# Performance work log

Measured on AMD Instinct MI355X. Metric: run time of the kernel, lower is better.

Reference implementation:

```python
import jax, jax.numpy as jnp
import numpy as np

B, T, D, H = 4, 2048, 384, 6
HD = D // H  # 64
HALF = HD // 2


def setup_inputs() -> dict:
    key = jax.random.key(0)
    k0, k1, k2 = jax.random.split(key, 3)
    x = jax.random.normal(k0, (B, T, D), jnp.float32)
    attn_bias = jnp.zeros((1, 1, T, T), jnp.float32)  # additive SDPA bias
    # standard RoPE tables: [T, HD/2]
    inv_freq = 1.0 / (10000.0 ** (np.arange(HALF, dtype=np.float32) / HALF))
    ang = np.arange(T, dtype=np.float32)[:, None] * inv_freq[None, :]
    cos = jnp.asarray(np.cos(ang), jnp.float32)
    sin = jnp.asarray(np.sin(ang), jnp.float32)
    w_qkv = jax.random.normal(k1, (D, 3 * D), jnp.float32) * (D ** -0.5)
    w_proj = jax.random.normal(k2, (D, D), jnp.float32) * (D ** -0.5)
    return {"x": x, "attn_bias": attn_bias, "cos": cos, "sin": sin,
            "w_qkv": w_qkv, "w_proj": w_proj}


def _apply_rope(x, cos, sin):
    # x: [b, h, t, hd]; cos/sin: [t, hd/2] -> rotate-half RoPE
    half = x.shape[-1] // 2
    x1, x2 = x[..., :half], x[..., half:]
    c = cos[None, None, :, :]
    s = sin[None, None, :, :]
    return jnp.concatenate([x1 * c - x2 * s, x2 * c + x1 * s], axis=-1)


def reference(x, attn_bias, cos, sin, w_qkv, w_proj):
    b, t, _ = x.shape
    qkv = (x @ w_qkv).reshape(b, t, 3, H, HD)  # fused QKV projection
    q = jnp.transpose(qkv[:, :, 0], (0, 2, 1, 3))  # [b,h,t,hd]
    k = jnp.transpose(qkv[:, :, 1], (0, 2, 1, 3))
    v = jnp.transpose(qkv[:, :, 2], (0, 2, 1, 3))
    q = _apply_rope(q, cos, sin)
    k = _apply_rope(k, cos, sin)
    scale = 1.0 / jnp.sqrt(jnp.asarray(HD, x.dtype))
    scores = jnp.einsum("bhqd,bhkd->bhqk", q, k) * scale + attn_bias
    attn = jax.nn.softmax(scores, axis=-1)
    out = jnp.einsum("bhqk,bhkd->bhqd", attn, v)
    out = jnp.transpose(out, (0, 2, 1, 3)).reshape(b, t, H * HD)
    return out @ w_proj
```

## Files before the change

### kernel.cpp

```cpp
#include <hip/hip_runtime.h>
#include <hip/hip_bf16.h>

#define BB   4
#define TT   2048
#define DDIM 384
#define HH   6
#define HD   64
#define BT   (BB*TT)
#define QKVC (3*DDIM)

#define QSCALE 0.18033688011112042f
#define LOG2E  1.4426950408889634f

typedef __attribute__((ext_vector_type(4))) short short4v;
typedef __attribute__((ext_vector_type(8))) short short8v;
typedef __attribute__((ext_vector_type(4))) float float4v;
typedef unsigned short u16;

static __device__ __forceinline__ u16 f2bu(float f) {
    __hip_bfloat16 h = __float2bfloat16(f);
    return __builtin_bit_cast(u16, h);
}
static __device__ __forceinline__ unsigned pk2(float lo, float hi) {
    return (unsigned)f2bu(lo) | ((unsigned)f2bu(hi) << 16);
}
static __device__ __forceinline__ short8v frag4(uint4 v) {
    return __builtin_bit_cast(short8v, v);
}
static __device__ __forceinline__ short8v ld_frag(const u16* p) {
    short4v a = *(const short4v*)p;
    short4v b = *(const short4v*)(p + 4);
    return __builtin_shufflevector(a, b, 0, 1, 2, 3, 4, 5, 6, 7);
}
static __device__ __forceinline__ void st8(u16* p, uint4 v) {
    *(uint2*)p       = make_uint2(v.x, v.y);
    *(uint2*)(p + 4) = make_uint2(v.z, v.w);
}
static __device__ __forceinline__ void pl32swap(unsigned &a, unsigned &b) {
    auto r = __builtin_amdgcn_permlane32_swap(a, b, false, false);
    a = r[0]; b = r[1];
}
static __device__ __forceinline__ void pl16swap(unsigned &a, unsigned &b) {
    auto r = __builtin_amdgcn_permlane16_swap(a, b, false, false);
    a = r[0]; b = r[1];
}

#define MFMA16(a, b, c) __builtin_amdgcn_mfma_f32_16x16x32_bf16((a), (b), (c), 0, 0, 0)

__global__ __launch_bounds__(256) void prep_kernel(
    const float* __restrict__ wqkv, const float* __restrict__ wproj,
    const float* __restrict__ x, const float* __restrict__ bias,
    u16* __restrict__ wqkvT, u16* __restrict__ wprojT,
    u16* __restrict__ xb, unsigned* __restrict__ flag)
{
    const int bid = blockIdx.x;
    const int t = threadIdx.x;
    if (bid >= 912) {
        const float* gp = bias + (size_t)(bid - 912) * 4096 + (size_t)t * 16;
        unsigned acc = 0;
        #pragma unroll
        for (int u = 0; u < 4; ++u) {
            float4 v = *(const float4*)(gp + 4 * u);
            acc |= (__builtin_bit_cast(unsigned, v.x) & 0x7fffffffu);
            acc |= (__builtin_bit_cast(unsigned, v.y) & 0x7fffffffu);
            acc |= (__builtin_bit_cast(unsigned, v.z) & 0x7fffffffu);
            acc |= (__builtin_bit_cast(unsigned, v.w) & 0x7fffffffu);
        }
        if (acc) atomicOr(flag, 1u);
        return;
    }
    if (bid >= 144) {
        size_t base = (size_t)(bid - 144) * 4096 + (size_t)t * 16;
        const float* gp = x + base;
        __align__(16) u16 tmp[16];
        #pragma unroll
        for (int u = 0; u < 4; ++u) {
            float4 v = *(const float4*)(gp + 4 * u);
            tmp[4 * u + 0] = f2bu(v.x); tmp[4 * u + 1] = f2bu(v.y);
            tmp[4 * u + 2] = f2bu(v.z); tmp[4 * u + 3] = f2bu(v.w);
        }
        *(uint4*)(xb + base)     = *(const uint4*)tmp;
        *(uint4*)(xb + base + 8) = *(const uint4*)(tmp + 8);
        return;
    }
    const float* in; u16* out; int K, C, c0, k0;
    if (bid < 108) { in = wqkv;  out = wqkvT;  K = DDIM; C = QKVC;
                     c0 = (bid % 18) * 64; k0 = (bid / 18) * 64; }
    else           { int b2 = bid - 108; in = wproj; out = wprojT; K = DDIM; C = DDIM;
                     c0 = (b2 % 6) * 64; k0 = (b2 / 6) * 64; }
    __shared__ float tr[64][65];
    {
        int kr = t >> 2, cb = (t & 3) * 16;
        const float* gp = in + (size_t)(k0 + kr) * C + c0 + cb;
        #pragma unroll
        for (int u = 0; u < 4; ++u) {
            float4 v = *(const float4*)(gp + 4 * u);
            tr[cb + 4 * u + 0][kr] = v.x;
            tr[cb + 4 * u + 1][kr] = v.y;
            tr[cb + 4 * u + 2][kr] = v.z;
            tr[cb + 4 * u + 3][kr] = v.w;
        }
    }
    __syncthreads();
    {
        int c = t >> 2, kb = (t & 3) * 16;
        __align__(16) u16 tmp[16];
        #pragma unroll
        for (int u = 0; u < 16; ++u) tmp[u] = f2bu(tr[c][kb + u]);
        u16* op = out + (size_t)(c0 + c) * K + k0 + kb;
        *(uint4*)op       = *(const uint4*)tmp;
        *(uint4*)(op + 8) = *(const uint4*)(tmp + 8);
    }
}

__global__ __launch_bounds__(256, 3) void qkv_rope_kernel(
    const u16* __restrict__ xb, const u16* __restrict__ wt,
    const float* __restrict__ cs, const float* __restrict__ sn,
    u16* __restrict__ qb, u16* __restrict__ kb, u16* __restrict__ vtb)
{
    __shared__ __align__(16) u16 ws[64][392];
    const int t = threadIdx.x;
    const int wv = t >> 6, lane = t & 63, quad = lane >> 4, lo = lane & 15;
    const int r0 = blockIdx.y * 64, c0 = blockIdx.x * 64;

    {
        const uint4* src = (const uint4*)(wt + (size_t)c0 * DDIM);
        #pragma unroll
        for (int u = 0; u < 12; ++u) {
            int idx = t + u * 256;
            int f = idx * 8;
            int row = f / DDIM, col = f % DDIM;
            *(uint4*)&ws[row][col] = src[idx];
        }
    }
    const u16* arow = xb + (size_t)(r0 + 16 * wv + lo) * DDIM + quad * 8;
    uint4 af[12];
    #pragma unroll
    for (int kf = 0; kf < 12; ++kf)
        af[kf] = *(const uint4*)(arow + kf * 32);
    __syncthreads();

    float4v acc[4] = {};
    #pragma unroll
    for (int kf = 0; kf < 12; ++kf) {
        short8v a = frag4(af[kf]);
        #pragma unroll
        for (int nt = 0; nt < 4; ++nt) {
            short8v b = ld_frag(&ws[nt * 16 + lo][kf * 32 + quad * 8]);
            acc[nt] = MFMA16(a, b, acc[nt]);
        }
    }

    const int sec = blockIdx.x / 6;
    const int h   = blockIdx.x % 6;
    const int rbase = r0 + 16 * wv + 4 * quad;
    const int bidx  = r0 >> 11;
    const int tbase = rbase & (TT - 1);

    if (sec == 2) {
        #pragma unroll
        for (int nt = 0; nt < 4; ++nt) {
            int d = nt * 16 + lo;
            unsigned a0 = pk2(acc[nt][0], acc[nt][1]);
            unsigned a1 = pk2(acc[nt][2], acc[nt][3]);
            u16* gp = vtb + ((size_t)(bidx * HH + h) * HD + d) * TT + tbase;
            *(uint2*)gp = make_uint2(a0, a1);
        }
    } else {
        u16* dst = (sec == 0) ? qb : kb;
        const float scl = (sec == 0) ? QSCALE : 1.0f;
        #pragma unroll
        for (int np = 0; np < 2; ++np) {
            #pragma unroll
            for (int r = 0; r < 4; ++r) {
                int tpos = tbase + r;
                int ci = np * 16 + lo;
                float cv = cs[tpos * 32 + ci];
                float sv = sn[tpos * 32 + ci];
                float x1 = acc[np][r], x2 = acc[np + 2][r];
                u16* gp = dst + ((size_t)(bidx * HH + h) * TT + tpos) * HD;
                gp[ci]      = f2bu((x1 * cv - x2 * sv) * scl);
                gp[ci + 32] = f2bu((x2 * cv + x1 * sv) * scl);
            }
        }
    }
}

__global__ __launch_bounds__(256, 2) void attn_ksplit_kernel(
    const u16* __restrict__ qb, const u16* __restrict__ kb, const u16* __restrict__ vtb,
    const unsigned* __restrict__ flag, u16* __restrict__ ob)
{
    if (*flag != 0u) return;

    __shared__ __align__(16) float red_o[2][64][68];
    __shared__ float red_l[4][64];

    const int t = threadIdx.x;
    const int wv = t >> 6, lane = t & 63, quad = lane >> 4, lo = lane & 15;
    const int bh = blockIdx.x;
    const int b = bh / HH, h = bh % HH;
    const int q0 = blockIdx.y * 64;

    short8v aq[4][2];
    #pragma unroll
    for (int g = 0; g < 4; ++g) {
        const u16* qp = qb + ((size_t)bh * TT + q0 + g * 16 + lo) * HD + quad * 8;
        aq[g][0] = frag4(*(const uint4*)qp);
        aq[g][1] = frag4(*(const uint4*)(qp + 32));
    }

    const u16* kbase = kb + ((size_t)bh * TT + lo) * HD + quad * 8;
    const u16* vbase = vtb + ((size_t)bh * HD + lo) * TT + quad * 8;

    uint4 kq[4][2], vq[4][2];
    {
        const size_t ko = (size_t)wv * 64 * HD;
        const size_t vo = (size_t)wv * 64;
        #pragma unroll
        for (int nt = 0; nt < 4; ++nt) {
            kq[nt][0] = *(const uint4*)(kbase + ko + (size_t)nt * 16 * HD);
            kq[nt][1] = *(const uint4*)(kbase + ko + (size_t)nt * 16 * HD + 32);
        }
        #pragma unroll
        for (int dt = 0; dt < 4; ++dt) {
            vq[dt][0] = *(const uint4*)(vbase + (size_t)dt * 16 * TT + vo);
            vq[dt][1] = *(const uint4*)(vbase + (size_t)dt * 16 * TT + vo + 32);
        }
    }

    float4v oacc[4][4] = {};
    float lacc[4] = {0.f, 0.f, 0.f, 0.f};

    for (int j = 0; j < 8; ++j) {
        const int ktn = (j < 7) ? (wv + 4 * (j + 1)) : wv;
        const size_t kno = (size_t)ktn * 64 * HD;
        const size_t vno = (size_t)ktn * 64;

        #pragma unroll
        for (int g = 0; g < 4; ++g) {
            float4v s[4] = {};
            #pragma unroll
            for (int nt = 0; nt < 4; ++nt)
                s[nt] = MFMA16(frag4(kq[nt][0]), aq[g][0], s[nt]);
            #pragma unroll
            for (int nt = 0; nt < 4; ++nt)
                s[nt] = MFMA16(frag4(kq[nt][1]), aq[g][1], s[nt]);
            if (g == 3) {
                #pragma unroll
                for (int nt = 0; nt < 4; ++nt) {
                    kq[nt][0] = *(const uint4*)(kbase + kno + (size_t)nt * 16 * HD);
                    kq[nt][1] = *(const uint4*)(kbase + kno + (size_t)nt * 16 * HD + 32);
                }
            }

            unsigned w[8];
            #pragma unroll
            for (int nt = 0; nt < 4; ++nt) {
                float p0 = __builtin_amdgcn_exp2f(s[nt][0]);
                float p1 = __builtin_amdgcn_exp2f(s[nt][1]);
                float p2 = __builtin_amdgcn_exp2f(s[nt][2]);
                float p3 = __builtin_amdgcn_exp2f(s[nt][3]);
                lacc[g] += (p0 + p1) + (p2 + p3);
                w[2 * nt]     = pk2(p0, p1);
                w[2 * nt + 1] = pk2(p2, p3);
            }

            pl32swap(w[0], w[2]); pl16swap(w[0], w[2]);
            pl32swap(w[1], w[3]); pl16swap(w[1], w[3]);
            pl32swap(w[4], w[6]); pl16swap(w[4], w[6]);
            pl32swap(w[5], w[7]); pl16swap(w[5], w[7]);
            short8v pa0 = frag4(make_uint4(w[0], w[1], w[2], w[3]));
            short8v pa1 = frag4(make_uint4(w[4], w[5], w[6], w[7]));

            #pragma unroll
            for (int dt = 0; dt < 4; ++dt)
                oacc[g][dt] = MFMA16(pa0, frag4(vq[dt][0]), oacc[g][dt]);
            #pragma unroll
            for (int dt = 0; dt < 4; ++dt)
                oacc[g][dt] = MFMA16(pa1, frag4(vq[dt][1]), oacc[g][dt]);
            if (g == 3) {
                #pragma unroll
                for (int dt = 0; dt < 4; ++dt) {
                    vq[dt][0] = *(const uint4*)(vbase + (size_t)dt * 16 * TT + vno);
                    vq[dt][1] = *(const uint4*)(vbase + (size_t)dt * 16 * TT + vno + 32);
                }
            }
        }
    }

    #pragma unroll
    for (int g = 0; g < 4; ++g) {
        lacc[g] += __shfl_xor(lacc[g], 16);
        lacc[g] += __shfl_xor(lacc[g], 32);
    }
    if (quad == 0) {
        #pragma unroll
        for (int g = 0; g < 4; ++g) red_l[wv][g * 16 + lo] = lacc[g];
    }
    float* slot0 = &red_o[0][0][0] + (size_t)lane * 68;
    float* slot1 = &red_o[1][0][0] + (size_t)lane * 68;
    if (wv == 1 || wv == 3) {
        float* sp = (wv == 1) ? slot0 : slot1;
        #pragma unroll
        for (int g = 0; g < 4; ++g)
            #pragma unroll
            for (int dt = 0; dt < 4; ++dt)
                *(float4v*)(sp + (g * 4 + dt) * 4) = oacc[g][dt];
    }
    __syncthreads();
    if (wv == 0 || wv == 2) {
        float* sp = (wv == 0) ? slot0 : slot1;
        #pragma unroll
        for (int g = 0; g < 4; ++g)
            #pragma unroll
            for (int dt = 0; dt < 4; ++dt)
                oacc[g][dt] += *(const float4v*)(sp + (g * 4 + dt) * 4);
    }
    __syncthreads();
    if (wv == 2) {
        #pragma unroll
        for (int g = 0; g < 4; ++g)
            #pragma unroll
            for (int dt = 0; dt < 4; ++dt)
                *(float4v*)(slot1 + (g * 4 + dt) * 4) = oacc[g][dt];
    }
    __syncthreads();
    if (wv == 0) {
        #pragma unroll
        for (int g = 0; g < 4; ++g) {
            #pragma unroll
            for (int dt = 0; dt < 4; ++dt)
                oacc[g][dt] += *(const float4v*)(slot1 + (g * 4 + dt) * 4);
            float lt = red_l[0][g * 16 + lo] + red_l[1][g * 16 + lo]
                     + red_l[2][g * 16 + lo] + red_l[3][g * 16 + lo];
            #pragma unroll
            for (int r = 0; r < 4; ++r) {
                float lr = __shfl(lt, 4 * quad + r);
                float inv = 1.f / lr;
                u16* gp = ob + ((size_t)b * TT + q0 + g * 16 + 4 * quad + r) * DDIM
                             + h * HD + lo;
                #pragma unroll
                for (int dt = 0; dt < 4; ++dt)
                    gp[dt * 16] = f2bu(oacc[g][dt][r] * inv);
            }
        }
    }
}

__global__ __launch_bounds__(256, 4) void attn_bias_kernel(
    const u16* __restrict__ qb, const u16* __restrict__ kb, const u16* __restrict__ vtb,
    const float* __restrict__ bias, const unsigned* __restrict__ flag,
    u16* __restrict__ ob)
{
    if (*flag == 0u) return;

    __shared__ __align__(16) u16 ks[2][64][68];
    __shared__ __align__(16) u16 vt[2][64][68];

    const int t = threadIdx.x;
    const int wv = t >> 6, lane = t & 63, quad = lane >> 4, lo = lane & 15;
    const int bh = blockIdx.x;
    const int b = bh / HH, h = bh % HH;
    const int q0 = blockIdx.y * 64;
    const int qrow = q0 + 16 * wv + lo;

    const u16* qbase = qb + ((size_t)bh * TT + qrow) * HD + quad * 8;
    short8v aq0 = frag4(*(const uint4*)qbase);
    short8v aq1 = frag4(*(const uint4*)(qbase + 32));

    const int sr = t >> 3, sd = (t & 7) * 8;
    const u16* kbbase = kb + (size_t)bh * TT * HD;
    const u16* vtbase = vtb + (size_t)bh * HD * TT;
    const float* brow = bias + (size_t)qrow * TT + 4 * quad;

    st8(&ks[0][sr][sd],      *(const uint4*)(kbbase + (size_t)sr * HD + sd));
    st8(&ks[0][sr + 32][sd], *(const uint4*)(kbbase + (size_t)(sr + 32) * HD + sd));
    st8(&vt[0][sr][sd],      *(const uint4*)(vtbase + (size_t)sr * TT + sd));
    st8(&vt[0][sr + 32][sd], *(const uint4*)(vtbase + (size_t)(sr + 32) * TT + sd));
    float4 bcur[4];
    #pragma unroll
    for (int nt = 0; nt < 4; ++nt) bcur[nt] = *(const float4*)(brow + nt * 16);
    __syncthreads();

    float4v oacc[4] = {};
    float lacc[4] = {0.f, 0.f, 0.f, 0.f};

    for (int kt = 0; kt < TT / 64; ++kt) {
        const int cur = kt & 1, nxt = cur ^ 1;
        const int kn = (kt < 31 ? kt + 1 : 31) * 64;

        uint4 kp0 = *(const uint4*)(kbbase + (size_t)(kn + sr) * HD + sd);
        uint4 kp1 = *(const uint4*)(kbbase + (size_t)(kn + sr + 32) * HD + sd);
        uint4 vp0 = *(const uint4*)(vtbase + (size_t)sr * TT + kn + sd);
        uint4 vp1 = *(const uint4*)(vtbase + (size_t)(sr + 32) * TT + kn + sd);
        float4 bnxt[4];
        #pragma unroll
        for (int nt = 0; nt < 4; ++nt) bnxt[nt] = *(const float4*)(brow + kn + nt * 16);

        float4v s[4] = {};
        #pragma unroll
        for (int kf = 0; kf < 2; ++kf) {
            #pragma unroll
            for (int nt = 0; nt < 4; ++nt) {
                short8v kfr = ld_frag(&ks[cur][nt * 16 + lo][kf * 32 + quad * 8]);
                s[nt] = MFMA16(kfr, (kf ? aq1 : aq0), s[nt]);
            }
        }

        unsigned w[8];
        #pragma unroll
        for (int nt = 0; nt < 4; ++nt) {
            float p0 = __builtin_amdgcn_exp2f(fmaf(bcur[nt].x, LOG2E, s[nt][0]));
            float p1 = __builtin_amdgcn_exp2f(fmaf(bcur[nt].y, LOG2E, s[nt][1]));
            float p2 = __builtin_amdgcn_exp2f(fmaf(bcur[nt].z, LOG2E, s[nt][2]));
            float p3 = __builtin_amdgcn_exp2f(fmaf(bcur[nt].w, LOG2E, s[nt][3]));
            lacc[nt] += (p0 + p1) + (p2 + p3);
            w[2 * nt]     = pk2(p0, p1);
            w[2 * nt + 1] = pk2(p2, p3);
        }

        pl32swap(w[0], w[2]); pl16swap(w[0], w[2]);
        pl32swap(w[1], w[3]); pl16swap(w[1], w[3]);
        pl32swap(w[4], w[6]); pl16swap(w[4], w[6]);
        pl32swap(w[5], w[7]); pl16swap(w[5], w[7]);
        short8v pa0 = frag4(make_uint4(w[0], w[1], w[2], w[3]));
        short8v pa1 = frag4(make_uint4(w[4], w[5], w[6], w[7]));

        #pragma unroll
        for (int kf = 0; kf < 2; ++kf) {
            #pragma unroll
            for (int dt = 0; dt < 4; ++dt) {
                short8v bv = ld_frag(&vt[cur][dt * 16 + lo][kf * 32 + quad * 8]);
                oacc[dt] = MFMA16((kf ? pa1 : pa0), bv, oacc[dt]);
            }
        }

        st8(&ks[nxt][sr][sd], kp0);
        st8(&ks[nxt][sr + 32][sd], kp1);
        st8(&vt[nxt][sr][sd], vp0);
        st8(&vt[nxt][sr + 32][sd], vp1);
        #pragma unroll
        for (int nt = 0; nt < 4; ++nt) bcur[nt] = bnxt[nt];
        __syncthreads();
    }

    float l = (lacc[0] + lacc[1]) + (lacc[2] + lacc[3]);
    l += __shfl_xor(l, 16);
    l += __shfl_xor(l, 32);
    #pragma unroll
    for (int r = 0; r < 4; ++r) {
        float lr = __shfl(l, 4 * quad + r);
        float inv = 1.f / lr;
        u16* gp = ob + ((size_t)b * TT + q0 + 16 * wv + 4 * quad + r) * DDIM + h * HD + lo;
        #pragma unroll
        for (int dt = 0; dt < 4; ++dt)
            gp[dt * 16] = f2bu(oacc[dt][r] * inv);
    }
}

__global__ __launch_bounds__(256, 3) void proj_kernel(
    const u16* __restrict__ o, const u16* __restrict__ wt, float* __restrict__ out)
{
    __shared__ __align__(16) u16 ws[64][392];
    const int t = threadIdx.x;
    const int wv = t >> 6, lane = t & 63, quad = lane >> 4, lo = lane & 15;
    const int r0 = blockIdx.y * 64, c0 = blockIdx.x * 64;

    {
        const uint4* src = (const uint4*)(wt + (size_t)c0 * DDIM);
        #pragma unroll
        for (int u = 0; u < 12; ++u) {
            int idx = t + u * 256;
            int f = idx * 8;
            int row = f / DDIM, col = f % DDIM;
            *(uint4*)&ws[row][col] = src[idx];
        }
    }
    const u16* arow = o + (size_t)(r0 + 16 * wv + lo) * DDIM + quad * 8;
    uint4 af[12];
    #pragma unroll
    for (int kf = 0; kf < 12; ++kf)
        af[kf] = *(const uint4*)(arow + kf * 32);
    __syncthreads();

    float4v acc[4] = {};
    #pragma unroll
    for (int kf = 0; kf < 12; ++kf) {
        short8v a = frag4(af[kf]);
        #pragma unroll
        for (int nt = 0; nt < 4; ++nt) {
            short8v b = ld_frag(&ws[nt * 16 + lo][kf * 32 + quad * 8]);
            acc[nt] = MFMA16(a, b, acc[nt]);
        }
    }
    #pragma unroll
    for (int r = 0; r < 4; ++r) {
        float* gp = out + (size_t)(r0 + 16 * wv + 4 * quad + r) * DDIM + c0;
        #pragma unroll
        for (int nt = 0; nt < 4; ++nt)
            gp[nt * 16 + lo] = acc[nt][r];
    }
}

extern "C" void kernel_launch(void* const* d_in, const int* in_sizes, int n_in,
                              void* d_out, int out_size, void* d_ws, size_t ws_size,
                              hipStream_t stream) {
    const float* x     = (const float*)d_in[0];
    const float* bias  = (const float*)d_in[1];
    const float* cs    = (const float*)d_in[2];
    const float* sn    = (const float*)d_in[3];
    const float* wqkv  = (const float*)d_in[4];
    const float* wproj = (const float*)d_in[5];
    float* out = (float*)d_out;

    u16* wqkvT  = (u16*)d_ws;
    u16* wprojT = wqkvT + (size_t)QKVC * DDIM;
    u16* qb     = wprojT + (size_t)DDIM * DDIM;
    u16* kb     = qb + (size_t)BB * HH * TT * HD;
    u16* vtb    = kb + (size_t)BB * HH * TT * HD;
    u16* ob     = vtb + (size_t)BB * HH * TT * HD;
    u16* xb     = ob + (size_t)BT * DDIM;
    unsigned* flag = (unsigned*)(xb + (size_t)BT * DDIM);

    hipMemsetAsync(flag, 0, sizeof(unsigned), stream);
    prep_kernel<<<dim3(144 + BT * DDIM / 4096 + TT * TT / 4096), 256, 0, stream>>>(
        wqkv, wproj, x, bias, wqkvT, wprojT, xb, flag);
    qkv_rope_kernel<<<dim3(QKVC / 64, BT / 64), 256, 0, stream>>>(
        xb, wqkvT, cs, sn, qb, kb, vtb);
    attn_ksplit_kernel<<<dim3(BB * HH, TT / 64), 256, 0, stream>>>(
        qb, kb, vtb, flag, ob);
    attn_bias_kernel<<<dim3(BB * HH, TT / 64), 256, 0, stream>>>(
        qb, kb, vtb, bias, flag, ob);
    proj_kernel<<<dim3(DDIM / 64, BT / 64), 256, 0, stream>>>(ob, wprojT, out);
}
```

Measured before the change: 171.7 us.

## Fuse fp32-to-bf16 weight and input conversion into GEMM kernels, merge attention kernels

Removes the separate prep kernel. The QKV and projection kernels now read fp32 weights and x directly, transposing and converting them to bf16 while staging into shared memory or registers. The bias-check blocks are appended to the QKV grid, and the two attention kernels are merged into one that branches on the flag, which saves a launch. In exchange, every GEMM block re-converts its weight tile from strided fp32 loads, so global traffic per block goes up.

```diff
diff --git a/kernel.cpp b/kernel.cpp
--- a/kernel.cpp
+++ b/kernel.cpp
@@ -47,16 +47,39 @@
 
 #define MFMA16(a, b, c) __builtin_amdgcn_mfma_f32_16x16x32_bf16((a), (b), (c), 0, 0, 0)
 
-__global__ __launch_bounds__(256) void prep_kernel(
-    const float* __restrict__ wqkv, const float* __restrict__ wproj,
-    const float* __restrict__ x, const float* __restrict__ bias,
-    u16* __restrict__ wqkvT, u16* __restrict__ wprojT,
-    u16* __restrict__ xb, unsigned* __restrict__ flag)
+static __device__ __forceinline__ void stage_wT(
+    u16 (*ws)[392], const float* __restrict__ w, int C, int c0, int t)
+{
+    const int c = t & 63;
+    const int kb0 = t >> 6;
+    #pragma unroll
+    for (int u = 0; u < 12; ++u) {
+        int k = (kb0 + 4 * u) * 8;
+        const float* wp = w + (size_t)k * C + c0 + c;
+        float v0 = wp[0];
+        float v1 = wp[(size_t)1 * C];
+        float v2 = wp[(size_t)2 * C];
+        float v3 = wp[(size_t)3 * C];
+        float v4 = wp[(size_t)4 * C];
+        float v5 = wp[(size_t)5 * C];
+        float v6 = wp[(size_t)6 * C];
+        float v7 = wp[(size_t)7 * C];
+        uint4 pv = make_uint4(pk2(v0, v1), pk2(v2, v3), pk2(v4, v5), pk2(v6, v7));
+        *(uint4*)&ws[c][k] = pv;
+    }
+}
+
+__global__ __launch_bounds__(256, 3) void qkv_fused_kernel(
+    const float* __restrict__ x, const float* __restrict__ wqkv,
+    const float* __restrict__ bias,
+    const float* __restrict__ cs, const float* __restrict__ sn,
+    u16* __restrict__ qb, u16* __restrict__ kb, u16* __restrict__ vtb,
+    unsigned* __restrict__ flag)
 {
     const int bid = blockIdx.x;
     const int t = threadIdx.x;
-    if (bid >= 912) {
-        const float* gp = bias + (size_t)(bid - 912) * 4096 + (size_t)t * 16;
+    if (bid >= 2304) {
+        const float* gp = bias + (size_t)(bid - 2304) * 4096 + (size_t)t * 16;
         unsigned acc = 0;
         #pragma unroll
         for (int u = 0; u < 4; ++u) {
@@ -69,75 +92,23 @@
         if (acc) atomicOr(flag, 1u);
         return;
     }
-    if (bid >= 144) {
-        size_t base = (size_t)(bid - 144) * 4096 + (size_t)t * 16;
-        const float* gp = x + base;
-        __align__(16) u16 tmp[16];
-        #pragma unroll
-        for (int u = 0; u < 4; ++u) {
-            float4 v = *(const float4*)(gp + 4 * u);
-            tmp[4 * u + 0] = f2bu(v.x); tmp[4 * u + 1] = f2bu(v.y);
-            tmp[4 * u + 2] = f2bu(v.z); tmp[4 * u + 3] = f2bu(v.w);
-        }
-        *(uint4*)(xb + base)     = *(const uint4*)tmp;
-        *(uint4*)(xb + base + 8) = *(const uint4*)(tmp + 8);
-        return;
-    }
-    const float* in; u16* out; int K, C, c0, k0;
-    if (bid < 108) { in = wqkv;  out = wqkvT;  K = DDIM; C = QKVC;
-                     c0 = (bid % 18) * 64; k0 = (bid / 18) * 64; }
-    else           { int b2 = bid - 108; in = wproj; out = wprojT; K = DDIM; C = DDIM;
-                     c0 = (b2 % 6) * 64; k0 = (b2 / 6) * 64; }
-    __shared__ float tr[64][65];
-    {
-        int kr = t >> 2, cb = (t & 3) * 16;
-        const float* gp = in + (size_t)(k0 + kr) * C + c0 + cb;
-        #pragma unroll
-        for (int u = 0; u < 4; ++u) {
-            float4 v = *(const float4*)(gp + 4 * u);
-            tr[cb + 4 * u + 0][kr] = v.x;
-            tr[cb + 4 * u + 1][kr] = v.y;
-            tr[cb + 4 * u + 2][kr] = v.z;
-            tr[cb + 4 * u + 3][kr] = v.w;
-        }
-    }
-    __syncthreads();
-    {
-        int c = t >> 2, kb = (t & 3) * 16;
-        __align__(16) u16 tmp[16];
-        #pragma unroll
-        for (int u = 0; u < 16; ++u) tmp[u] = f2bu(tr[c][kb + u]);
-        u16* op = out + (size_t)(c0 + c) * K + k0 + kb;
-        *(uint4*)op       = *(const uint4*)tmp;
-        *(uint4*)(op + 8) = *(const uint4*)(tmp + 8);
-    }
-}
-
-__global__ __launch_bounds__(256, 3) void qkv_rope_kernel(
-    const u16* __restrict__ xb, const u16* __restrict__ wt,
-    const float* __restrict__ cs, const float* __restrict__ sn,
-    u16* __restrict__ qb, u16* __restrict__ kb, u16* __restrict__ vtb)
-{
+
     __shared__ __align__(16) u16 ws[64][392];
-    const int t = threadIdx.x;
     const int wv = t >> 6, lane = t & 63, quad = lane >> 4, lo = lane & 15;
-    const int r0 = blockIdx.y * 64, c0 = blockIdx.x * 64;
-
-    {
-        const uint4* src = (const uint4*)(wt + (size_t)c0 * DDIM);
-        #pragma unroll
-        for (int u = 0; u < 12; ++u) {
-            int idx = t + u * 256;
-            int f = idx * 8;
-            int row = f / DDIM, col = f % DDIM;
-            *(uint4*)&ws[row][col] = src[idx];
-        }
-    }
-    const u16* arow = xb + (size_t)(r0 + 16 * wv + lo) * DDIM + quad * 8;
+    const int c0 = (bid % 18) * 64;
+    const int r0 = (bid / 18) * 64;
+
+    stage_wT(ws, wqkv, QKVC, c0, t);
+
+    const float* arow = x + (size_t)(r0 + 16 * wv + lo) * DDIM + quad * 8;
     uint4 af[12];
     #pragma unroll
-    for (int kf = 0; kf < 12; ++kf)
-        af[kf] = *(const uint4*)(arow + kf * 32);
+    for (int kf = 0; kf < 12; ++kf) {
+        float4 a0 = *(const float4*)(arow + kf * 32);
+        float4 a1 = *(const float4*)(arow + kf * 32 + 4);
+        af[kf] = make_uint4(pk2(a0.x, a0.y), pk2(a0.z, a0.w),
+                            pk2(a1.x, a1.y), pk2(a1.z, a1.w));
+    }
     __syncthreads();
 
     float4v acc[4] = {};
@@ -151,8 +122,9 @@
         }
     }
 
-    const int sec = blockIdx.x / 6;
-    const int h   = blockIdx.x % 6;
+    const int cb = bid % 18;
+    const int sec = cb / 6;
+    const int h   = cb % 6;
     const int rbase = r0 + 16 * wv + 4 * quad;
     const int bidx  = r0 >> 11;
     const int tbase = rbase & (TT - 1);
@@ -186,14 +158,12 @@
     }
 }
 
-__global__ __launch_bounds__(256, 2) void attn_ksplit_kernel(
+__global__ __launch_bounds__(256, 2) void attn_unified_kernel(
     const u16* __restrict__ qb, const u16* __restrict__ kb, const u16* __restrict__ vtb,
-    const unsigned* __restrict__ flag, u16* __restrict__ ob)
+    const float* __restrict__ bias, const unsigned* __restrict__ flag,
+    u16* __restrict__ ob)
 {
-    if (*flag != 0u) return;
-
-    __shared__ __align__(16) float red_o[2][64][68];
-    __shared__ float red_l[4][64];
+    __shared__ __align__(16) u16 smem[17920];
 
     const int t = threadIdx.x;
     const int wv = t >> 6, lane = t & 63, quad = lane >> 4, lo = lane & 15;
@@ -201,66 +171,215 @@
     const int b = bh / HH, h = bh % HH;
     const int q0 = blockIdx.y * 64;
 
-    short8v aq[4][2];
-    #pragma unroll
-    for (int g = 0; g < 4; ++g) {
-        const u16* qp = qb + ((size_t)bh * TT + q0 + g * 16 + lo) * HD + quad * 8;
-        aq[g][0] = frag4(*(const uint4*)qp);
-        aq[g][1] = frag4(*(const uint4*)(qp + 32));
-    }
-
-    const u16* kbase = kb + ((size_t)bh * TT + lo) * HD + quad * 8;
-    const u16* vbase = vtb + ((size_t)bh * HD + lo) * TT + quad * 8;
-
-    uint4 kq[4][2], vq[4][2];
+    if (*flag == 0u) {
+        float* red_o = (float*)smem;
+        float* red_l = (float*)(smem + 17408);
+
+        short8v aq[4][2];
+        #pragma unroll
+        for (int g = 0; g < 4; ++g) {
+            const u16* qp = qb + ((size_t)bh * TT + q0 + g * 16 + lo) * HD + quad * 8;
+            aq[g][0] = frag4(*(const uint4*)qp);
+            aq[g][1] = frag4(*(const uint4*)(qp + 32));
+        }
+
+        const u16* kbase = kb + ((size_t)bh * TT + lo) * HD + quad * 8;
+        const u16* vbase = vtb + ((size_t)bh * HD + lo) * TT + quad * 8;
+
+        uint4 kq[4][2], vq[4][2];
+        {
+            const size_t ko = (size_t)wv * 64 * HD;
+            const size_t vo = (size_t)wv * 64;
+            #pragma unroll
+            for (int nt = 0; nt < 4; ++nt) {
+                kq[nt][0] = *(const uint4*)(kbase + ko + (size_t)nt * 16 * HD);
+                kq[nt][1] = *(const uint4*)(kbase + ko + (size_t)nt * 16 * HD + 32);
+            }
+            #pragma unroll
+            for (int dt = 0; dt < 4; ++dt) {
+                vq[dt][0] = *(const uint4*)(vbase + (size_t)dt * 16 * TT + vo);
+                vq[dt][1] = *(const uint4*)(vbase + (size_t)dt * 16 * TT + vo + 32);
+            }
+        }
+
+        float4v oacc[4][4] = {};
+        float lacc[4] = {0.f, 0.f, 0.f, 0.f};
+
+        for (int j = 0; j < 8; ++j) {
+            const int ktn = (j < 7) ? (wv + 4 * (j + 1)) : wv;
+            const size_t kno = (size_t)ktn * 64 * HD;
+            const size_t vno = (size_t)ktn * 64;
+
+            #pragma unroll
+            for (int g = 0; g < 4; ++g) {
+                float4v s[4] = {};
+                #pragma unroll
+                for (int nt = 0; nt < 4; ++nt)
+                    s[nt] = MFMA16(frag4(kq[nt][0]), aq[g][0], s[nt]);
+                #pragma unroll
+                for (int nt = 0; nt < 4; ++nt)
+                    s[nt] = MFMA16(frag4(kq[nt][1]), aq[g][1], s[nt]);
+                if (g == 3) {
+                    #pragma unroll
+                    for (int nt = 0; nt < 4; ++nt) {
+                        kq[nt][0] = *(const uint4*)(kbase + kno + (size_t)nt * 16 * HD);
+                        kq[nt][1] = *(const uint4*)(kbase + kno + (size_t)nt * 16 * HD + 32);
+                    }
+                }
+
+                unsigned w[8];
+                #pragma unroll
+                for (int nt = 0; nt < 4; ++nt) {
+                    float p0 = __builtin_amdgcn_exp2f(s[nt][0]);
+                    float p1 = __builtin_amdgcn_exp2f(s[nt][1]);
+                    float p2 = __builtin_amdgcn_exp2f(s[nt][2]);
+                    float p3 = __builtin_amdgcn_exp2f(s[nt][3]);
+                    lacc[g] += (p0 + p1) + (p2 + p3);
+                    w[2 * nt]     = pk2(p0, p1);
+                    w[2 * nt + 1] = pk2(p2, p3);
+                }
+
+                pl32swap(w[0], w[2]); pl16swap(w[0], w[2]);
+                pl32swap(w[1], w[3]); pl16swap(w[1], w[3]);
+                pl32swap(w[4], w[6]); pl16swap(w[4], w[6]);
+                pl32swap(w[5], w[7]); pl16swap(w[5], w[7]);
+                short8v pa0 = frag4(make_uint4(w[0], w[1], w[2], w[3]));
+                short8v pa1 = frag4(make_uint4(w[4], w[5], w[6], w[7]));
+
+                #pragma unroll
+                for (int dt = 0; dt < 4; ++dt)
+                    oacc[g][dt] = MFMA16(pa0, frag4(vq[dt][0]), oacc[g][dt]);
+                #pragma unroll
+                for (int dt = 0; dt < 4; ++dt)
+                    oacc[g][dt] = MFMA16(pa1, frag4(vq[dt][1]), oacc[g][dt]);
+                if (g == 3) {
+                    #pragma unroll
+                    for (int dt = 0; dt < 4; ++dt) {
+                        vq[dt][0] = *(const uint4*)(vbase + (size_t)dt * 16 * TT + vno);
+                        vq[dt][1] = *(const uint4*)(vbase + (size_t)dt * 16 * TT + vno + 32);
+                    }
+                }
+            }
+        }
+
+        #pragma unroll
+        for (int g = 0; g < 4; ++g) {
+            lacc[g] += __shfl_xor(lacc[g], 16);
+            lacc[g] += __shfl_xor(lacc[g], 32);
+        }
+        if (quad == 0) {
+            #pragma unroll
+            for (int g = 0; g < 4; ++g) red_l[wv * 64 + g * 16 + lo] = lacc[g];
+        }
+        float* slot0 = red_o + (size_t)lane * 68;
+        float* slot1 = red_o + 64 * 68 + (size_t)lane * 68;
+        if (wv == 1 || wv == 3) {
+            float* sp = (wv == 1) ? slot0 : slot1;
+            #pragma unroll
+            for (int g = 0; g < 4; ++g)
+                #pragma unroll
+                for (int dt = 0; dt < 4; ++dt)
+                    *(float4v*)(sp + (g * 4 + dt) * 4) = oacc[g][dt];
+        }
+        __syncthreads();
+        if (wv == 0 || wv == 2) {
+            float* sp = (wv == 0) ? slot0 : slot1;
+            #pragma unroll
+            for (int g = 0; g < 4; ++g)
+                #pragma unroll
+                for (int dt = 0; dt < 4; ++dt)
+                    oacc[g][dt] += *(const float4v*)(sp + (g * 4 + dt) * 4);
+        }
+        __syncthreads();
+        if (wv == 2) {
+            #pragma unroll
+            for (int g = 0; g < 4; ++g)
+                #pragma unroll
+                for (int dt = 0; dt < 4; ++dt)
+                    *(float4v*)(slot1 + (g * 4 + dt) * 4) = oacc[g][dt];
+        }
+        __syncthreads();
+        if (wv == 0) {
+            #pragma unroll
+            for (int g = 0; g < 4; ++g) {
+                #pragma unroll
+                for (int dt = 0; dt < 4; ++dt)
+                    oacc[g][dt] += *(const float4v*)(slot1 + (g * 4 + dt) * 4);
+                float lt = red_l[0 * 64 + g * 16 + lo] + red_l[1 * 64 + g * 16 + lo]
+                         + red_l[2 * 64 + g * 16 + lo] + red_l[3 * 64 + g * 16 + lo];
+                #pragma unroll
+                for (int r = 0; r < 4; ++r) {
+                    float lr = __shfl(lt, 4 * quad + r);
+                    float inv = 1.f / lr;
+                    u16* gp = ob + ((size_t)b * TT + q0 + g * 16 + 4 * quad + r) * DDIM
+                                 + h * HD + lo;
+                    #pragma unroll
+                    for (int dt = 0; dt < 4; ++dt)
+                        gp[dt * 16] = f2bu(oacc[g][dt][r] * inv);
+                }
+            }
+        }
+        return;
+    }
+
     {
-        const size_t ko = (size_t)wv * 64 * HD;
-        const size_t vo = (size_t)wv * 64;
-        #pragma unroll
-        for (int nt = 0; nt < 4; ++nt) {
-            kq[nt][0] = *(const uint4*)(kbase + ko + (size_t)nt * 16 * HD);
-            kq[nt][1] = *(const uint4*)(kbase + ko + (size_t)nt * 16 * HD + 32);
-        }
-        #pragma unroll
-        for (int dt = 0; dt < 4; ++dt) {
-            vq[dt][0] = *(const uint4*)(vbase + (size_t)dt * 16 * TT + vo);
-            vq[dt][1] = *(const uint4*)(vbase + (size_t)dt * 16 * TT + vo + 32);
-        }
-    }
-
-    float4v oacc[4][4] = {};
-    float lacc[4] = {0.f, 0.f, 0.f, 0.f};
-
-    for (int j = 0; j < 8; ++j) {
-        const int ktn = (j < 7) ? (wv + 4 * (j + 1)) : wv;
-        const size_t kno = (size_t)ktn * 64 * HD;
-        const size_t vno = (size_t)ktn * 64;
-
-        #pragma unroll
-        for (int g = 0; g < 4; ++g) {
+        typedef u16 (*lds_t)[64][68];
+        lds_t ks = (lds_t)smem;
+        lds_t vt = (lds_t)(smem + 8704);
+
+        const int qrow = q0 + 16 * wv + lo;
+        const u16* qbase = qb + ((size_t)bh * TT + qrow) * HD + quad * 8;
+        short8v aq0 = frag4(*(const uint4*)qbase);
+        short8v aq1 = frag4(*(const uint4*)(qbase + 32));
+
+        const int sr = t >> 3, sd = (t & 7) * 8;
+        const u16* kbbase = kb + (size_t)bh * TT * HD;
+        const u16* vtbase = vtb + (size_t)bh * HD * TT;
+        const float* brow = bias + (size_t)qrow * TT + 4 * quad;
+
+        st8(&ks[0][sr][sd],      *(const uint4*)(kbbase + (size_t)sr * HD + sd));
+        st8(&ks[0][sr + 32][sd], *(const uint4*)(kbbase + (size_t)(sr + 32) * HD + sd));
+        st8(&vt[0][sr][sd],      *(const uint4*)(vtbase + (size_t)sr * TT + sd));
+        st8(&vt[0][sr + 32][sd], *(const uint4*)(vtbase + (size_t)(sr + 32) * TT + sd));
+        float4 bcur[4];
+        #pragma unroll
+        for (int nt = 0; nt < 4; ++nt) bcur[nt] = *(const float4*)(brow + nt * 16);
+        __syncthreads();
+
+        float4v oacc[4] = {};
+        float lacc[4] = {0.f, 0.f, 0.f, 0.f};
+
+        for (int kt = 0; kt < TT / 64; ++kt) {
+            const int cur = kt & 1, nxt = cur ^ 1;
+            const int kn = (kt < 31 ? kt + 1 : 31) * 64;
+
+            uint4 kp0 = *(const uint4*)(kbbase + (size_t)(kn + sr) * HD + sd);
+            uint4 kp1 = *(const uint4*)(kbbase + (size_t)(kn + sr + 32) * HD + sd);
+            uint4 vp0 = *(const uint4*)(vtbase + (size_t)sr * TT + kn + sd);
+            uint4 vp1 = *(const uint4*)(vtbase + (size_t)(sr + 32) * TT + kn + sd);
+            float4 bnxt[4];
+            #pragma unroll
+            for (int nt = 0; nt < 4; ++nt)
+                bnxt[nt] = *(const float4*)(brow + kn + nt * 16);
+
             float4v s[4] = {};
             #pragma unroll
-            for (int nt = 0; nt < 4; ++nt)
-                s[nt] = MFMA16(frag4(kq[nt][0]), aq[g][0], s[nt]);
-            #pragma unroll
-            for (int nt = 0; nt < 4; ++nt)
-                s[nt] = MFMA16(frag4(kq[nt][1]), aq[g][1], s[nt]);
-            if (g == 3) {
+            for (int kf = 0; kf < 2; ++kf) {
                 #pragma unroll
                 for (int nt = 0; nt < 4; ++nt) {
-                    kq[nt][0] = *(const uint4*)(kbase + kno + (size_t)nt * 16 * HD);
-                    kq[nt][1] = *(const uint4*)(kbase + kno + (size_t)nt * 16 * HD + 32);
+                    short8v kfr = ld_frag(&ks[cur][nt * 16 + lo][kf * 32 + quad * 8]);
+                    s[nt] = MFMA16(kfr, (kf ? aq1 : aq0), s[nt]);
                 }
             }
 
             unsigned w[8];
             #pragma unroll
             for (int nt = 0; nt < 4; ++nt) {
-                float p0 = __builtin_amdgcn_exp2f(s[nt][0]);
-                float p1 = __builtin_amdgcn_exp2f(s[nt][1]);
-                float p2 = __builtin_amdgcn_exp2f(s[nt][2]);
-                float p3 = __builtin_amdgcn_exp2f(s[nt][3]);
-                lacc[g] += (p0 + p1) + (p2 + p3);
+                float p0 = __builtin_amdgcn_exp2f(fmaf(bcur[nt].x, LOG2E, s[nt][0]));
+                float p1 = __builtin_amdgcn_exp2f(fmaf(bcur[nt].y, LOG2E, s[nt][1]));
+                float p2 = __builtin_amdgcn_exp2f(fmaf(bcur[nt].z, LOG2E, s[nt][2]));
+                float p3 = __builtin_amdgcn_exp2f(fmaf(bcur[nt].w, LOG2E, s[nt][3]));
+                lacc[nt] += (p0 + p1) + (p2 + p3);
                 w[2 * nt]     = pk2(p0, p1);
                 w[2 * nt + 1] = pk2(p2, p3);
             }
@@ -273,209 +392,50 @@
             short8v pa1 = frag4(make_uint4(w[4], w[5], w[6], w[7]));
 
             #pragma unroll
+            for (int kf = 0; kf < 2; ++kf) {
+                #pragma unroll
+                for (int dt = 0; dt < 4; ++dt) {
+                    short8v bv = ld_frag(&vt[cur][dt * 16 + lo][kf * 32 + quad * 8]);
+                    oacc[dt] = MFMA16((kf ? pa1 : pa0), bv, oacc[dt]);
+                }
+            }
+
+            st8(&ks[nxt][sr][sd], kp0);
+            st8(&ks[nxt][sr + 32][sd], kp1);
+            st8(&vt[nxt][sr][sd], vp0);
+            st8(&vt[nxt][sr + 32][sd], vp1);
+            #pragma unroll
+            for (int nt = 0; nt < 4; ++nt) bcur[nt] = bnxt[nt];
+            __syncthreads();
+        }
+
+        float l = (lacc[0] + lacc[1]) + (lacc[2] + lacc[3]);
+        l += __shfl_xor(l, 16);
+        l += __shfl_xor(l, 32);
+        #pragma unroll
+        for (int r = 0; r < 4; ++r) {
+            float lr = __shfl(l, 4 * quad + r);
+            float inv = 1.f / lr;
+            u16* gp = ob + ((size_t)b * TT + q0 + 16 * wv + 4 * quad + r) * DDIM
+                         + h * HD + lo;
+            #pragma unroll
             for (int dt = 0; dt < 4; ++dt)
-                oacc[g][dt] = MFMA16(pa0, frag4(vq[dt][0]), oacc[g][dt]);
-            #pragma unroll
-            for (int dt = 0; dt < 4; ++dt)
-                oacc[g][dt] = MFMA16(pa1, frag4(vq[dt][1]), oacc[g][dt]);
-            if (g == 3) {
-                #pragma unroll
-                for (int dt = 0; dt < 4; ++dt) {
-                    vq[dt][0] = *(const uint4*)(vbase + (size_t)dt * 16 * TT + vno);
-                    vq[dt][1] = *(const uint4*)(vbase + (size_t)dt * 16 * TT + vno + 32);
-                }
-            }
-        }
-    }
-
-    #pragma unroll
-    for (int g = 0; g < 4; ++g) {
-        lacc[g] += __shfl_xor(lacc[g], 16);
-        lacc[g] += __shfl_xor(lacc[g], 32);
-    }
-    if (quad == 0) {
-        #pragma unroll
-        for (int g = 0; g < 4; ++g) red_l[wv][g * 16 + lo] = lacc[g];
-    }
-    float* slot0 = &red_o[0][0][0] + (size_t)lane * 68;
-    float* slot1 = &red_o[1][0][0] + (size_t)lane * 68;
-    if (wv == 1 || wv == 3) {
-        float* sp = (wv == 1) ? slot0 : slot1;
-        #pragma unroll
-        for (int g = 0; g < 4; ++g)
-            #pragma unroll
-            for (int dt = 0; dt < 4; ++dt)
-                *(float4v*)(sp + (g * 4 + dt) * 4) = oacc[g][dt];
-    }
-    __syncthreads();
-    if (wv == 0 || wv == 2) {
-        float* sp = (wv == 0) ? slot0 : slot1;
-        #pragma unroll
-        for (int g = 0; g < 4; ++g)
-            #pragma unroll
-            for (int dt = 0; dt < 4; ++dt)
-                oacc[g][dt] += *(const float4v*)(sp + (g * 4 + dt) * 4);
-    }
-    __syncthreads();
-    if (wv == 2) {
-        #pragma unroll
-        for (int g = 0; g < 4; ++g)
-            #pragma unroll
-            for (int dt = 0; dt < 4; ++dt)
-                *(float4v*)(slot1 + (g * 4 + dt) * 4) = oacc[g][dt];
-    }
-    __syncthreads();
-    if (wv == 0) {
-        #pragma unroll
-        for (int g = 0; g < 4; ++g) {
-            #pragma unroll
-            for (int dt = 0; dt < 4; ++dt)
-                oacc[g][dt] += *(const float4v*)(slot1 + (g * 4 + dt) * 4);
-            float lt = red_l[0][g * 16 + lo] + red_l[1][g * 16 + lo]
-                     + red_l[2][g * 16 + lo] + red_l[3][g * 16 + lo];
-            #pragma unroll
-            for (int r = 0; r < 4; ++r) {
-                float lr = __shfl(lt, 4 * quad + r);
-                float inv = 1.f / lr;
-                u16* gp = ob + ((size_t)b * TT + q0 + g * 16 + 4 * quad + r) * DDIM
-                             + h * HD + lo;
-                #pragma unroll
-                for (int dt = 0; dt < 4; ++dt)
-                    gp[dt * 16] = f2bu(oacc[g][dt][r] * inv);
-            }
-        }
-    }
-}
-
-__global__ __launch_bounds__(256, 4) void attn_bias_kernel(
-    const u16* __restrict__ qb, const u16* __restrict__ kb, const u16* __restrict__ vtb,
-    const float* __restrict__ bias, const unsigned* __restrict__ flag,
-    u16* __restrict__ ob)
-{
-    if (*flag == 0u) return;
-
-    __shared__ __align__(16) u16 ks[2][64][68];
-    __shared__ __align__(16) u16 vt[2][64][68];
-
-    const int t = threadIdx.x;
-    const int wv = t >> 6, lane = t & 63, quad = lane >> 4, lo = lane & 15;
-    const int bh = blockIdx.x;
-    const int b = bh / HH, h = bh % HH;
-    const int q0 = blockIdx.y * 64;
-    const int qrow = q0 + 16 * wv + lo;
-
-    const u16* qbase = qb + ((size_t)bh * TT + qrow) * HD + quad * 8;
-    short8v aq0 = frag4(*(const uint4*)qbase);
-    short8v aq1 = frag4(*(const uint4*)(qbase + 32));
-
-    const int sr = t >> 3, sd = (t & 7) * 8;
-    const u16* kbbase = kb + (size_t)bh * TT * HD;
-    const u16* vtbase = vtb + (size_t)bh * HD * TT;
-    const float* brow = bias + (size_t)qrow * TT + 4 * quad;
-
-    st8(&ks[0][sr][sd],      *(const uint4*)(kbbase + (size_t)sr * HD + sd));
-    st8(&ks[0][sr + 32][sd], *(const uint4*)(kbbase + (size_t)(sr + 32) * HD + sd));
-    st8(&vt[0][sr][sd],      *(const uint4*)(vtbase + (size_t)sr * TT + sd));
-    st8(&vt[0][sr + 32][sd], *(const uint4*)(vtbase + (size_t)(sr + 32) * TT + sd));
-    float4 bcur[4];
-    #pragma unroll
-    for (int nt = 0; nt < 4; ++nt) bcur[nt] = *(const float4*)(brow + nt * 16);
-    __syncthreads();
-
-    float4v oacc[4] = {};
-    float lacc[4] = {0.f, 0.f, 0.f, 0.f};
-
-    for (int kt = 0; kt < TT / 64; ++kt) {
-        const int cur = kt & 1, nxt = cur ^ 1;
-        const int kn = (kt < 31 ? kt + 1 : 31) * 64;
-
-        uint4 kp0 = *(const uint4*)(kbbase + (size_t)(kn + sr) * HD + sd);
-        uint4 kp1 = *(const uint4*)(kbbase + (size_t)(kn + sr + 32) * HD + sd);
-        uint4 vp0 = *(const uint4*)(vtbase + (size_t)sr * TT + kn + sd);
-        uint4 vp1 = *(const uint4*)(vtbase + (size_t)(sr + 32) * TT + kn + sd);
-        float4 bnxt[4];
-        #pragma unroll
-        for (int nt = 0; nt < 4; ++nt) bnxt[nt] = *(const float4*)(brow + kn + nt * 16);
-
-        float4v s[4] = {};
-        #pragma unroll
-        for (int kf = 0; kf < 2; ++kf) {
-            #pragma unroll
-            for (int nt = 0; nt < 4; ++nt) {
-                short8v kfr = ld_frag(&ks[cur][nt * 16 + lo][kf * 32 + quad * 8]);
-                s[nt] = MFMA16(kfr, (kf ? aq1 : aq0), s[nt]);
-            }
-        }
-
-        unsigned w[8];
-        #pragma unroll
-        for (int nt = 0; nt < 4; ++nt) {
-            float p0 = __builtin_amdgcn_exp2f(fmaf(bcur[nt].x, LOG2E, s[nt][0]));
-            float p1 = __builtin_amdgcn_exp2f(fmaf(bcur[nt].y, LOG2E, s[nt][1]));
-            float p2 = __builtin_amdgcn_exp2f(fmaf(bcur[nt].z, LOG2E, s[nt][2]));
-            float p3 = __builtin_amdgcn_exp2f(fmaf(bcur[nt].w, LOG2E, s[nt][3]));
-            lacc[nt] += (p0 + p1) + (p2 + p3);
-            w[2 * nt]     = pk2(p0, p1);
-            w[2 * nt + 1] = pk2(p2, p3);
-        }
-
-        pl32swap(w[0], w[2]); pl16swap(w[0], w[2]);
-        pl32swap(w[1], w[3]); pl16swap(w[1], w[3]);
-        pl32swap(w[4], w[6]); pl16swap(w[4], w[6]);
-        pl32swap(w[5], w[7]); pl16swap(w[5], w[7]);
-        short8v pa0 = frag4(make_uint4(w[0], w[1], w[2], w[3]));
-        short8v pa1 = frag4(make_uint4(w[4], w[5], w[6], w[7]));
-
-        #pragma unroll
-        for (int kf = 0; kf < 2; ++kf) {
-            #pragma unroll
-            for (int dt = 0; dt < 4; ++dt) {
-                short8v bv = ld_frag(&vt[cur][dt * 16 + lo][kf * 32 + quad * 8]);
-                oacc[dt] = MFMA16((kf ? pa1 : pa0), bv, oacc[dt]);
-            }
-        }
-
-        st8(&ks[nxt][sr][sd], kp0);
-        st8(&ks[nxt][sr + 32][sd], kp1);
-        st8(&vt[nxt][sr][sd], vp0);
-        st8(&vt[nxt][sr + 32][sd], vp1);
-        #pragma unroll
-        for (int nt = 0; nt < 4; ++nt) bcur[nt] = bnxt[nt];
-        __syncthreads();
-    }
-
-    float l = (lacc[0] + lacc[1]) + (lacc[2] + lacc[3]);
-    l += __shfl_xor(l, 16);
-    l += __shfl_xor(l, 32);
-    #pragma unroll
-    for (int r = 0; r < 4; ++r) {
-        float lr = __shfl(l, 4 * quad + r);
-        float inv = 1.f / lr;
-        u16* gp = ob + ((size_t)b * TT + q0 + 16 * wv + 4 * quad + r) * DDIM + h * HD + lo;
-        #pragma unroll
-        for (int dt = 0; dt < 4; ++dt)
-            gp[dt * 16] = f2bu(oacc[dt][r] * inv);
-    }
-}
-
-__global__ __launch_bounds__(256, 3) void proj_kernel(
-    const u16* __restrict__ o, const u16* __restrict__ wt, float* __restrict__ out)
+                gp[dt * 16] = f2bu(oacc[dt][r] * inv);
+        }
+    }
+}
+
+__global__ __launch_bounds__(256, 3) void proj_fused_kernel(
+    const u16* __restrict__ o, const float* __restrict__ wproj,
+    float* __restrict__ out)
 {
     __shared__ __align__(16) u16 ws[64][392];
     const int t = threadIdx.x;
     const int wv = t >> 6, lane = t & 63, quad = lane >> 4, lo = lane & 15;
     const int r0 = blockIdx.y * 64, c0 = blockIdx.x * 64;
 
-    {
-        const uint4* src = (const uint4*)(wt + (size_t)c0 * DDIM);
-        #pragma unroll
-        for (int u = 0; u < 12; ++u) {
-            int idx = t + u * 256;
-            int f = idx * 8;
-            int row = f / DDIM, col = f % DDIM;
-            *(uint4*)&ws[row][col] = src[idx];
-        }
-    }
+    stage_wT(ws, wproj, DDIM, c0, t);
+
     const u16* arow = o + (size_t)(r0 + 16 * wv + lo) * DDIM + quad * 8;
     uint4 af[12];
     #pragma unroll
@@ -513,23 +473,17 @@
     const float* wproj = (const float*)d_in[5];
     float* out = (float*)d_out;
 
-    u16* wqkvT  = (u16*)d_ws;
-    u16* wprojT = wqkvT + (size_t)QKVC * DDIM;
-    u16* qb     = wprojT + (size_t)DDIM * DDIM;
-    u16* kb     = qb + (size_t)BB * HH * TT * HD;
-    u16* vtb    = kb + (size_t)BB * HH * TT * HD;
-    u16* ob     = vtb + (size_t)BB * HH * TT * HD;
-    u16* xb     = ob + (size_t)BT * DDIM;
-    unsigned* flag = (unsigned*)(xb + (size_t)BT * DDIM);
+    u16* qb  = (u16*)d_ws;
+    u16* kb  = qb + (size_t)BB * HH * TT * HD;
+    u16* vtb = kb + (size_t)BB * HH * TT * HD;
+    u16* ob  = vtb + (size_t)BB * HH * TT * HD;
+    unsigned* flag = (unsigned*)(ob + (size_t)BT * DDIM);
 
     hipMemsetAsync(flag, 0, sizeof(unsigned), stream);
-    prep_kernel<<<dim3(144 + BT * DDIM / 4096 + TT * TT / 4096), 256, 0, stream>>>(
-        wqkv, wproj, x, bias, wqkvT, wprojT, xb, flag);
-    qkv_rope_kernel<<<dim3(QKVC / 64, BT / 64), 256, 0, stream>>>(
-        xb, wqkvT, cs, sn, qb, kb, vtb);
-    attn_ksplit_kernel<<<dim3(BB * HH, TT / 64), 256, 0, stream>>>(
-        qb, kb, vtb, flag, ob);
-    attn_bias_kernel<<<dim3(BB * HH, TT / 64), 256, 0, stream>>>(
+    qkv_fused_kernel<<<2304 + TT * TT / 4096, 256, 0, stream>>>(
+        x, wqkv, bias, cs, sn, qb, kb, vtb, flag);
+    attn_unified_kernel<<<dim3(BB * HH, TT / 64), 256, 0, stream>>>(
         qb, kb, vtb, bias, flag, ob);
-    proj_kernel<<<dim3(DDIM / 64, BT / 64), 256, 0, stream>>>(ob, wprojT, out);
-}
+    proj_fused_kernel<<<dim3(DDIM / 64, BT / 64), 256, 0, stream>>>(
+        ob, wproj, out);
+}
```

New measurement: 177.6 us. 3.4% more time.
